# Kernel optimization log

Measured on AMD Instinct MI355X. Metric: run time of the kernel, lower is better.

Reference implementation:

```python
import jax, jax.numpy as jnp
import numpy as np

N = 8192   # nodes
D = 128    # uniform feature dim (arch = [128,128,128])
L = 2      # num_layers = len(arch)-1
EDGE_P = 0.01

def setup_inputs() -> dict:
    key = jax.random.key(0)
    ks = jax.random.split(key, 11)
    features = jax.random.normal(ks[0], (N, D), dtype=jnp.float32)
    # sparse symmetric adjacency with self-loops (diagonal forced True, as in forward)
    a = jax.random.uniform(ks[1], (N, N)) < EDGE_P
    mask = a | a.T | jnp.eye(N, dtype=bool)
    s = 1.0 / np.sqrt(D)
    def w(k):
        return (jax.random.normal(k, (L, D, D), dtype=jnp.float32) * s)
    def b(k):
        return jax.random.normal(k, (L, D), dtype=jnp.float32) * 0.01
    return {
        "features": features, "mask": mask,
        "Wq": w(ks[2]), "bq": b(ks[3]),
        "Wk": w(ks[4]), "bk": b(ks[5]),
        "Wv": w(ks[6]), "bv": b(ks[7]),
        "Wo": w(ks[8]), "bo": b(ks[9]),
    }

def reference(features, mask, Wq, bq, Wk, bk, Wv, bv, Wo, bo):
    h = features
    outputs = [h]
    for l in range(L):
        Q = h @ Wq[l] + bq[l]                      # [N, D]
        K = h @ Wk[l] + bk[l]
        V = h @ Wv[l] + bv[l]
        scores = (Q @ K.T) * (1.0 / jnp.sqrt(jnp.float32(K.shape[1])))  # [N, N]
        scores = jnp.where(mask, scores, -jnp.inf)
        attn = jax.nn.softmax(scores, axis=1)
        h = attn @ V                                # [N, D]
        h = h @ Wo[l] + bo[l]
        outputs.append(h)
    return tuple(outputs)
```

## Files before the change

kernel.cpp:

```cpp
#include <hip/hip_runtime.h>
#include <hip/hip_bf16.h>
#include <hip/hip_fp16.h>
#include <math.h>

#define N 8192
#define D 128
#define CAP 512

typedef _Float16 f16x2 __attribute__((ext_vector_type(2)));
typedef _Float16 f16x4 __attribute__((ext_vector_type(4)));
typedef _Float16 f16x8 __attribute__((ext_vector_type(8)));
typedef float    f32x4 __attribute__((ext_vector_type(4)));

__device__ __forceinline__ float dot2(f16x2 a, f16x2 b, float c) {
#if __has_builtin(__builtin_amdgcn_fdot2)
    return __builtin_amdgcn_fdot2(a, b, c, false);
#else
    return c + (float)a[0] * (float)b[0] + (float)a[1] * (float)b[1];
#endif
}

__device__ __forceinline__ float dot8(f16x8 a, f16x8 b) {
    float c0 = dot2(__builtin_shufflevector(a, a, 0, 1), __builtin_shufflevector(b, b, 0, 1), 0.f);
    float c1 = dot2(__builtin_shufflevector(a, a, 2, 3), __builtin_shufflevector(b, b, 2, 3), 0.f);
    c0 = dot2(__builtin_shufflevector(a, a, 4, 5), __builtin_shufflevector(b, b, 4, 5), c0);
    c1 = dot2(__builtin_shufflevector(a, a, 6, 7), __builtin_shufflevector(b, b, 6, 7), c1);
    return c0 + c1;
}

__global__ __launch_bounds__(256) void adj_qkv(const int* __restrict__ mask,
                                               unsigned short* __restrict__ nbr,
                                               int* __restrict__ deg,
                                               const float* __restrict__ A,
                                               const float* __restrict__ Wq, const float* __restrict__ bq,
                                               const float* __restrict__ Wk, const float* __restrict__ bk,
                                               const float* __restrict__ Wv, const float* __restrict__ bv,
                                               __half* __restrict__ Qo, __half* __restrict__ Ko,
                                               __half* __restrict__ Vo,
                                               float* __restrict__ copy_out) {
    __shared__ float As[8][D];
    const int tid = threadIdx.x;

    if (blockIdx.x < N) {
        const int i = blockIdx.x;
        __shared__ int cnt;
        if (tid == 0) cnt = 0;
        __syncthreads();
        const int4* row = (const int4*)(mask + (size_t)i * N);
        for (int c = tid; c < N / 4; c += 256) {
            int4 m4 = row[c];
            int base = 4 * c;
            if (m4.x) { int p = atomicAdd(&cnt, 1); if (p < CAP) nbr[(size_t)i * CAP + p] = (unsigned short)(base); }
            if (m4.y) { int p = atomicAdd(&cnt, 1); if (p < CAP) nbr[(size_t)i * CAP + p] = (unsigned short)(base + 1); }
            if (m4.z) { int p = atomicAdd(&cnt, 1); if (p < CAP) nbr[(size_t)i * CAP + p] = (unsigned short)(base + 2); }
            if (m4.w) { int p = atomicAdd(&cnt, 1); if (p < CAP) nbr[(size_t)i * CAP + p] = (unsigned short)(base + 3); }
        }
        __syncthreads();
        if (tid == 0) deg[i] = (cnt > CAP) ? CAP : cnt;
        return;
    }

    const int r   = tid >> 5;
    const int jg  = tid & 31;
    const int i0  = (blockIdx.x - N) * 8;

    const float4 av = ((const float4*)(A + (size_t)i0 * D))[tid];
    ((float4*)&As[0][0])[tid] = av;
    ((float4*)(copy_out + (size_t)i0 * D))[tid] = av;
    __syncthreads();

    const float* Ws[3] = {Wq, Wk, Wv};
    const float* bs[3] = {bq, bk, bv};
    __half* Os[3] = {Qo, Ko, Vo};
    const size_t st[3] = {D, 2 * D, 2 * D};

    #pragma unroll
    for (int m = 0; m < 3; ++m) {
        float4 acc = *(const float4*)(bs[m] + 4 * jg);
        const float* W = Ws[m];
        #pragma unroll 8
        for (int k4 = 0; k4 < 32; ++k4) {
            const float4 a4 = *(const float4*)&As[r][4 * k4];
            const float* wb = W + (size_t)(4 * k4) * D + 4 * jg;
            const float4 w0 = *(const float4*)(wb);
            const float4 w1 = *(const float4*)(wb + D);
            const float4 w2 = *(const float4*)(wb + 2 * D);
            const float4 w3 = *(const float4*)(wb + 3 * D);
            acc.x += a4.x * w0.x + a4.y * w1.x + a4.z * w2.x + a4.w * w3.x;
            acc.y += a4.x * w0.y + a4.y * w1.y + a4.z * w2.y + a4.w * w3.y;
            acc.z += a4.x * w0.z + a4.y * w1.z + a4.z * w2.z + a4.w * w3.z;
            acc.w += a4.x * w0.w + a4.y * w1.w + a4.z * w2.w + a4.w * w3.w;
        }
        f16x4 h;
        h[0] = (_Float16)acc.x; h[1] = (_Float16)acc.y;
        h[2] = (_Float16)acc.z; h[3] = (_Float16)acc.w;
        *(f16x4*)(Os[m] + (size_t)(i0 + r) * st[m] + 4 * jg) = h;
    }
}

__global__ __launch_bounds__(256) void gemmO_qkv(const float* __restrict__ Aattn,
                                                 const float* __restrict__ Wo, const float* __restrict__ bo,
                                                 float* __restrict__ Hout,
                                                 const float* __restrict__ Wq, const float* __restrict__ bq,
                                                 const float* __restrict__ Wk, const float* __restrict__ bk,
                                                 const float* __restrict__ Wv, const float* __restrict__ bv,
                                                 __half* __restrict__ Qo, __half* __restrict__ Ko,
                                                 __half* __restrict__ Vo) {
    __shared__ float As[8][D];
    __shared__ float Hs[8][D];
    const int tid = threadIdx.x;
    const int r   = tid >> 5;
    const int jg  = tid & 31;
    const int i0  = blockIdx.x * 8;

    ((float4*)&As[0][0])[tid] = ((const float4*)(Aattn + (size_t)i0 * D))[tid];
    __syncthreads();

    {
        float4 acc = *(const float4*)(bo + 4 * jg);
        #pragma unroll 8
        for (int k4 = 0; k4 < 32; ++k4) {
            const float4 a4 = *(const float4*)&As[r][4 * k4];
            const float* wb = Wo + (size_t)(4 * k4) * D + 4 * jg;
            const float4 w0 = *(const float4*)(wb);
            const float4 w1 = *(const float4*)(wb + D);
            const float4 w2 = *(const float4*)(wb + 2 * D);
            const float4 w3 = *(const float4*)(wb + 3 * D);
            acc.x += a4.x * w0.x + a4.y * w1.x + a4.z * w2.x + a4.w * w3.x;
            acc.y += a4.x * w0.y + a4.y * w1.y + a4.z * w2.y + a4.w * w3.y;
            acc.z += a4.x * w0.z + a4.y * w1.z + a4.z * w2.z + a4.w * w3.z;
            acc.w += a4.x * w0.w + a4.y * w1.w + a4.z * w2.w + a4.w * w3.w;
        }
        *(float4*)(Hout + (size_t)(i0 + r) * D + 4 * jg) = acc;
        *(float4*)&Hs[r][4 * jg] = acc;
    }
    __syncthreads();

    const float* Ws[3] = {Wq, Wk, Wv};
    const float* bs[3] = {bq, bk, bv};
    __half* Os[3] = {Qo, Ko, Vo};
    const size_t st[3] = {D, 2 * D, 2 * D};
    #pragma unroll
    for (int m = 0; m < 3; ++m) {
        float4 acc = *(const float4*)(bs[m] + 4 * jg);
        const float* W = Ws[m];
        #pragma unroll 8
        for (int k4 = 0; k4 < 32; ++k4) {
            const float4 a4 = *(const float4*)&Hs[r][4 * k4];
            const float* wb = W + (size_t)(4 * k4) * D + 4 * jg;
            const float4 w0 = *(const float4*)(wb);
            const float4 w1 = *(const float4*)(wb + D);
            const float4 w2 = *(const float4*)(wb + 2 * D);
            const float4 w3 = *(const float4*)(wb + 3 * D);
            acc.x += a4.x * w0.x + a4.y * w1.x + a4.z * w2.x + a4.w * w3.x;
            acc.y += a4.x * w0.y + a4.y * w1.y + a4.z * w2.y + a4.w * w3.y;
            acc.z += a4.x * w0.z + a4.y * w1.z + a4.z * w2.z + a4.w * w3.z;
            acc.w += a4.x * w0.w + a4.y * w1.w + a4.z * w2.w + a4.w * w3.w;
        }
        f16x4 h;
        h[0] = (_Float16)acc.x; h[1] = (_Float16)acc.y;
        h[2] = (_Float16)acc.z; h[3] = (_Float16)acc.w;
        *(f16x4*)(Os[m] + (size_t)(i0 + r) * st[m] + 4 * jg) = h;
    }
}

__global__ __launch_bounds__(256) void gemm_bias(const float* __restrict__ A,
                                                 const float* __restrict__ W,
                                                 const float* __restrict__ bias,
                                                 float* __restrict__ C) {
    __shared__ float As[8][D];
    const int tid = threadIdx.x;
    const int r   = tid >> 5;
    const int jg  = tid & 31;
    const int i0  = blockIdx.x * 8;

    ((float4*)&As[0][0])[tid] = ((const float4*)(A + (size_t)i0 * D))[tid];
    __syncthreads();

    float4 acc = *(const float4*)(bias + 4 * jg);
    #pragma unroll 8
    for (int k4 = 0; k4 < 32; ++k4) {
        const float4 a4 = *(const float4*)&As[r][4 * k4];
        const float* wb = W + (size_t)(4 * k4) * D + 4 * jg;
        const float4 w0 = *(const float4*)(wb);
        const float4 w1 = *(const float4*)(wb + D);
        const float4 w2 = *(const float4*)(wb + 2 * D);
        const float4 w3 = *(const float4*)(wb + 3 * D);
        acc.x += a4.x * w0.x + a4.y * w1.x + a4.z * w2.x + a4.w * w3.x;
        acc.y += a4.x * w0.y + a4.y * w1.y + a4.z * w2.y + a4.w * w3.y;
        acc.z += a4.x * w0.z + a4.y * w1.z + a4.z * w2.z + a4.w * w3.z;
        acc.w += a4.x * w0.w + a4.y * w1.w + a4.z * w2.w + a4.w * w3.w;
    }
    *(float4*)(C + (size_t)(i0 + r) * D + 4 * jg) = acc;
}

__global__ __launch_bounds__(256, 8) void attn_sparse(const __half* __restrict__ Q,
                                                      const __half* __restrict__ KV,
                                                      const unsigned short* __restrict__ nbr,
                                                      const int* __restrict__ deg,
                                                      float* __restrict__ Hout) {
    const int tid  = threadIdx.x;
    const int wave = tid >> 6;
    const int lane = tid & 63;
    const int g    = lane >> 4;
    const int gl   = lane & 15;
    const int i    = blockIdx.x * 4 + wave;

    __shared__ unsigned short jls[4][CAP];

    const int dg = min(deg[i], CAP);
    for (int e = lane; e < dg; e += 64)
        jls[wave][e] = __builtin_nontemporal_load(&nbr[(size_t)i * CAP + e]);
    const f16x8 qv = ((const f16x8*)(Q + (size_t)i * D))[gl];
    __syncthreads();

    const float scale = 0.088388347648318447f;

    float acc[8] = {0.f, 0.f, 0.f, 0.f, 0.f, 0.f, 0.f, 0.f};
    float denom  = 0.f;

    for (int e = g; e < dg; e += 4) {
        const int j = jls[wave][e];
        const f16x8* kvp = (const f16x8*)(KV + (size_t)j * (2 * D));
        const f16x8 kv = kvp[gl];
        const f16x8 v8 = kvp[16 + gl];
        float dot = dot8(kv, qv);
        dot += __shfl_xor(dot, 1);
        dot += __shfl_xor(dot, 2);
        dot += __shfl_xor(dot, 4);
        dot += __shfl_xor(dot, 8);
        const float p = __expf(dot * scale);
        #pragma unroll
        for (int k = 0; k < 8; ++k) acc[k] += p * (float)v8[k];
        denom += p;
    }

    #pragma unroll
    for (int k = 0; k < 8; ++k) {
        acc[k] += __shfl_xor(acc[k], 16);
        acc[k] += __shfl_xor(acc[k], 32);
    }
    denom += __shfl_xor(denom, 16);
    denom += __shfl_xor(denom, 32);

    if (g == 0) {
        const float inv = 1.0f / denom;
        f32x4 o0, o1;
        o0[0] = acc[0] * inv; o0[1] = acc[1] * inv; o0[2] = acc[2] * inv; o0[3] = acc[3] * inv;
        o1[0] = acc[4] * inv; o1[1] = acc[5] * inv; o1[2] = acc[6] * inv; o1[3] = acc[7] * inv;
        f32x4* dst = (f32x4*)(Hout + (size_t)i * D + 8 * gl);
        __builtin_nontemporal_store(o0, &dst[0]);
        __builtin_nontemporal_store(o1, &dst[1]);
    }
}

extern "C" void kernel_launch(void* const* d_in, const int* in_sizes, int n_in,
                              void* d_out, int out_size, void* d_ws, size_t ws_size,
                              hipStream_t stream) {
    const float* features = (const float*)d_in[0];
    const int*   mask     = (const int*)d_in[1];
    const float* Wq = (const float*)d_in[2];
    const float* bq = (const float*)d_in[3];
    const float* Wk = (const float*)d_in[4];
    const float* bk = (const float*)d_in[5];
    const float* Wv = (const float*)d_in[6];
    const float* bv = (const float*)d_in[7];
    const float* Wo = (const float*)d_in[8];
    const float* bo = (const float*)d_in[9];
    float* out = (float*)d_out;

    char* base = (char*)d_ws;
    unsigned short* nbr = (unsigned short*)base;
    int*    deg  = (int*)(base + (size_t)N * CAP * 2);
    __half* Qb16 = (__half*)(base + (size_t)N * CAP * 2 + N * 4);
    __half* KVb  = Qb16 + (size_t)N * D;
    float*  tmp  = (float*)(KVb + (size_t)N * 2 * D);

    adj_qkv<<<N + N / 8, 256, 0, stream>>>(mask, nbr, deg,
                                           features, Wq, bq, Wk, bk, Wv, bv,
                                           Qb16, KVb, KVb + D, out);
    attn_sparse<<<N / 4, 256, 0, stream>>>(Qb16, KVb, nbr, deg, tmp);
    gemmO_qkv<<<N / 8, 256, 0, stream>>>(tmp, Wo, bo, out + (size_t)N * D,
                                         Wq + D * D, bq + D, Wk + D * D, bk + D,
                                         Wv + D * D, bv + D, Qb16, KVb, KVb + D);
    attn_sparse<<<N / 4, 256, 0, stream>>>(Qb16, KVb, nbr, deg, tmp);
    gemm_bias<<<N / 8, 256, 0, stream>>>(tmp, Wo + D * D, bo + D,
                                         out + (size_t)2 * N * D);
}
```

Baseline: 569.3 us.

## Split sparse attention into two column-half passes for K/V cache locality

Neighbor lists are bucketed by whether the column lies in the first or second half of nodes, with per-half degrees. Attention runs as two passes, each gathering K/V only from one half so the working set per pass is halved and should hit cache more often. The first pass stores unnormalized partial sums and denominators, and the second combines and normalizes. This adds an extra kernel launch per layer and a global round trip for the partial accumulators, and caps each half at 256 neighbors.

```diff
diff --git a/kernel.cpp b/kernel.cpp
--- a/kernel.cpp
+++ b/kernel.cpp
@@ -6,6 +6,7 @@
 #define N 8192
 #define D 128
 #define CAP 512
+#define HCAP 256
 
 typedef _Float16 f16x2 __attribute__((ext_vector_type(2)));
 typedef _Float16 f16x4 __attribute__((ext_vector_type(4)));
@@ -30,7 +31,7 @@
 
 __global__ __launch_bounds__(256) void adj_qkv(const int* __restrict__ mask,
                                                unsigned short* __restrict__ nbr,
-                                               int* __restrict__ deg,
+                                               int* __restrict__ deg2,
                                                const float* __restrict__ A,
                                                const float* __restrict__ Wq, const float* __restrict__ bq,
                                                const float* __restrict__ Wk, const float* __restrict__ bk,
@@ -43,20 +44,22 @@
 
     if (blockIdx.x < N) {
         const int i = blockIdx.x;
-        __shared__ int cnt;
-        if (tid == 0) cnt = 0;
+        __shared__ int cnt2[2];
+        if (tid < 2) cnt2[tid] = 0;
         __syncthreads();
         const int4* row = (const int4*)(mask + (size_t)i * N);
         for (int c = tid; c < N / 4; c += 256) {
             int4 m4 = row[c];
             int base = 4 * c;
-            if (m4.x) { int p = atomicAdd(&cnt, 1); if (p < CAP) nbr[(size_t)i * CAP + p] = (unsigned short)(base); }
-            if (m4.y) { int p = atomicAdd(&cnt, 1); if (p < CAP) nbr[(size_t)i * CAP + p] = (unsigned short)(base + 1); }
-            if (m4.z) { int p = atomicAdd(&cnt, 1); if (p < CAP) nbr[(size_t)i * CAP + p] = (unsigned short)(base + 2); }
-            if (m4.w) { int p = atomicAdd(&cnt, 1); if (p < CAP) nbr[(size_t)i * CAP + p] = (unsigned short)(base + 3); }
+            int half = (base >= N / 2);
+            int boff = half * HCAP;
+            if (m4.x) { int p = atomicAdd(&cnt2[half], 1); if (p < HCAP) nbr[(size_t)i * CAP + boff + p] = (unsigned short)(base); }
+            if (m4.y) { int p = atomicAdd(&cnt2[half], 1); if (p < HCAP) nbr[(size_t)i * CAP + boff + p] = (unsigned short)(base + 1); }
+            if (m4.z) { int p = atomicAdd(&cnt2[half], 1); if (p < HCAP) nbr[(size_t)i * CAP + boff + p] = (unsigned short)(base + 2); }
+            if (m4.w) { int p = atomicAdd(&cnt2[half], 1); if (p < HCAP) nbr[(size_t)i * CAP + boff + p] = (unsigned short)(base + 3); }
         }
         __syncthreads();
-        if (tid == 0) deg[i] = (cnt > CAP) ? CAP : cnt;
+        if (tid < 2) deg2[2 * i + tid] = (cnt2[tid] > HCAP) ? HCAP : cnt2[tid];
         return;
     }
 
@@ -194,11 +197,14 @@
     *(float4*)(C + (size_t)(i0 + r) * D + 4 * jg) = acc;
 }
 
-__global__ __launch_bounds__(256, 8) void attn_sparse(const __half* __restrict__ Q,
-                                                      const __half* __restrict__ KV,
-                                                      const unsigned short* __restrict__ nbr,
-                                                      const int* __restrict__ deg,
-                                                      float* __restrict__ Hout) {
+template <int HALF>
+__global__ __launch_bounds__(256, 8) void attn_pass(const __half* __restrict__ Q,
+                                                    const __half* __restrict__ KV,
+                                                    const unsigned short* __restrict__ nbr,
+                                                    const int* __restrict__ deg2,
+                                                    float* __restrict__ Hacc,
+                                                    float* __restrict__ den,
+                                                    float* __restrict__ Hout) {
     const int tid  = threadIdx.x;
     const int wave = tid >> 6;
     const int lane = tid & 63;
@@ -206,12 +212,13 @@
     const int gl   = lane & 15;
     const int i    = blockIdx.x * 4 + wave;
 
-    __shared__ unsigned short jls[4][CAP];
-
-    const int dg = min(deg[i], CAP);
+    __shared__ unsigned short jls[4][HCAP];
+
+    const int dg = min(deg2[2 * i + HALF], HCAP);
+    const unsigned short* nb = nbr + (size_t)i * CAP + HALF * HCAP;
     for (int e = lane; e < dg; e += 64)
-        jls[wave][e] = __builtin_nontemporal_load(&nbr[(size_t)i * CAP + e]);
-    const f16x8 qv = ((const f16x8*)(Q + (size_t)i * D))[gl];
+        jls[wave][e] = __builtin_nontemporal_load(&nb[e]);
+    const f16x8 qv = __builtin_nontemporal_load(&((const f16x8*)(Q + (size_t)i * D))[gl]);
     __syncthreads();
 
     const float scale = 0.088388347648318447f;
@@ -243,14 +250,31 @@
     denom += __shfl_xor(denom, 16);
     denom += __shfl_xor(denom, 32);
 
-    if (g == 0) {
-        const float inv = 1.0f / denom;
-        f32x4 o0, o1;
-        o0[0] = acc[0] * inv; o0[1] = acc[1] * inv; o0[2] = acc[2] * inv; o0[3] = acc[3] * inv;
-        o1[0] = acc[4] * inv; o1[1] = acc[5] * inv; o1[2] = acc[6] * inv; o1[3] = acc[7] * inv;
-        f32x4* dst = (f32x4*)(Hout + (size_t)i * D + 8 * gl);
-        __builtin_nontemporal_store(o0, &dst[0]);
-        __builtin_nontemporal_store(o1, &dst[1]);
+    if constexpr (HALF == 0) {
+        if (g == 0) {
+            f32x4 o0, o1;
+            o0[0] = acc[0]; o0[1] = acc[1]; o0[2] = acc[2]; o0[3] = acc[3];
+            o1[0] = acc[4]; o1[1] = acc[5]; o1[2] = acc[6]; o1[3] = acc[7];
+            f32x4* dst = (f32x4*)(Hacc + (size_t)i * D + 8 * gl);
+            __builtin_nontemporal_store(o0, &dst[0]);
+            __builtin_nontemporal_store(o1, &dst[1]);
+        }
+        if (lane == 0) den[i] = denom;
+    } else {
+        if (g == 0) {
+            const f32x4* src = (const f32x4*)(Hacc + (size_t)i * D + 8 * gl);
+            const f32x4 a0 = __builtin_nontemporal_load(&src[0]);
+            const f32x4 a1 = __builtin_nontemporal_load(&src[1]);
+            const float inv = 1.0f / (denom + den[i]);
+            f32x4 o0, o1;
+            o0[0] = (acc[0] + a0[0]) * inv; o0[1] = (acc[1] + a0[1]) * inv;
+            o0[2] = (acc[2] + a0[2]) * inv; o0[3] = (acc[3] + a0[3]) * inv;
+            o1[0] = (acc[4] + a1[0]) * inv; o1[1] = (acc[5] + a1[1]) * inv;
+            o1[2] = (acc[6] + a1[2]) * inv; o1[3] = (acc[7] + a1[3]) * inv;
+            f32x4* dst = (f32x4*)(Hout + (size_t)i * D + 8 * gl);
+            __builtin_nontemporal_store(o0, &dst[0]);
+            __builtin_nontemporal_store(o1, &dst[1]);
+        }
     }
 }
 
@@ -271,19 +295,23 @@
 
     char* base = (char*)d_ws;
     unsigned short* nbr = (unsigned short*)base;
-    int*    deg  = (int*)(base + (size_t)N * CAP * 2);
-    __half* Qb16 = (__half*)(base + (size_t)N * CAP * 2 + N * 4);
+    int*    deg2 = (int*)(base + (size_t)N * CAP * 2);
+    float*  den  = (float*)(base + (size_t)N * CAP * 2 + 2 * N * 4);
+    __half* Qb16 = (__half*)(base + (size_t)N * CAP * 2 + 2 * N * 4 + N * 4);
     __half* KVb  = Qb16 + (size_t)N * D;
     float*  tmp  = (float*)(KVb + (size_t)N * 2 * D);
-
-    adj_qkv<<<N + N / 8, 256, 0, stream>>>(mask, nbr, deg,
+    float*  Hacc = out + (size_t)2 * N * D;
+
+    adj_qkv<<<N + N / 8, 256, 0, stream>>>(mask, nbr, deg2,
                                            features, Wq, bq, Wk, bk, Wv, bv,
                                            Qb16, KVb, KVb + D, out);
-    attn_sparse<<<N / 4, 256, 0, stream>>>(Qb16, KVb, nbr, deg, tmp);
+    attn_pass<0><<<N / 4, 256, 0, stream>>>(Qb16, KVb, nbr, deg2, Hacc, den, tmp);
+    attn_pass<1><<<N / 4, 256, 0, stream>>>(Qb16, KVb, nbr, deg2, Hacc, den, tmp);
     gemmO_qkv<<<N / 8, 256, 0, stream>>>(tmp, Wo, bo, out + (size_t)N * D,
                                          Wq + D * D, bq + D, Wk + D * D, bk + D,
                                          Wv + D * D, bv + D, Qb16, KVb, KVb + D);
-    attn_sparse<<<N / 4, 256, 0, stream>>>(Qb16, KVb, nbr, deg, tmp);
+    attn_pass<0><<<N / 4, 256, 0, stream>>>(Qb16, KVb, nbr, deg2, Hacc, den, tmp);
+    attn_pass<1><<<N / 4, 256, 0, stream>>>(Qb16, KVb, nbr, deg2, Hacc, den, tmp);
     gemm_bias<<<N / 8, 256, 0, stream>>>(tmp, Wo + D * D, bo + D,
                                          out + (size_t)2 * N * D);
 }
```

After: 584.2 us. 2.6% more time.

## Fuse output projection and next-layer QKV projection into sparse attention kernel

Applied to the files above, without the earlier changes.

The sparse attention kernel now also applies the Wo projection to each node's attention output. For the first layer it then computes the next layer's Q/K/V projections in the same kernel. This drops two separate GEMM launches and the fp32 intermediate round-trip through global memory. Each wave handles one row with a per-row matvec, so weight matrices are re-read once per 4-row block instead of once per 8-row block. Q/KV buffers are double-buffered to avoid overwriting inputs still being read by other blocks.

```diff
diff --git a/kernel.cpp b/kernel.cpp
--- a/kernel.cpp
+++ b/kernel.cpp
@@ -10,6 +10,7 @@
 typedef _Float16 f16x2 __attribute__((ext_vector_type(2)));
 typedef _Float16 f16x4 __attribute__((ext_vector_type(4)));
 typedef _Float16 f16x8 __attribute__((ext_vector_type(8)));
+typedef float    f32x2 __attribute__((ext_vector_type(2)));
 typedef float    f32x4 __attribute__((ext_vector_type(4)));
 
 __device__ __forceinline__ float dot2(f16x2 a, f16x2 b, float c) {
@@ -98,107 +99,18 @@
     }
 }
 
-__global__ __launch_bounds__(256) void gemmO_qkv(const float* __restrict__ Aattn,
-                                                 const float* __restrict__ Wo, const float* __restrict__ bo,
-                                                 float* __restrict__ Hout,
-                                                 const float* __restrict__ Wq, const float* __restrict__ bq,
-                                                 const float* __restrict__ Wk, const float* __restrict__ bk,
-                                                 const float* __restrict__ Wv, const float* __restrict__ bv,
-                                                 __half* __restrict__ Qo, __half* __restrict__ Ko,
-                                                 __half* __restrict__ Vo) {
-    __shared__ float As[8][D];
-    __shared__ float Hs[8][D];
-    const int tid = threadIdx.x;
-    const int r   = tid >> 5;
-    const int jg  = tid & 31;
-    const int i0  = blockIdx.x * 8;
-
-    ((float4*)&As[0][0])[tid] = ((const float4*)(Aattn + (size_t)i0 * D))[tid];
-    __syncthreads();
-
-    {
-        float4 acc = *(const float4*)(bo + 4 * jg);
-        #pragma unroll 8
-        for (int k4 = 0; k4 < 32; ++k4) {
-            const float4 a4 = *(const float4*)&As[r][4 * k4];
-            const float* wb = Wo + (size_t)(4 * k4) * D + 4 * jg;
-            const float4 w0 = *(const float4*)(wb);
-            const float4 w1 = *(const float4*)(wb + D);
-            const float4 w2 = *(const float4*)(wb + 2 * D);
-            const float4 w3 = *(const float4*)(wb + 3 * D);
-            acc.x += a4.x * w0.x + a4.y * w1.x + a4.z * w2.x + a4.w * w3.x;
-            acc.y += a4.x * w0.y + a4.y * w1.y + a4.z * w2.y + a4.w * w3.y;
-            acc.z += a4.x * w0.z + a4.y * w1.z + a4.z * w2.z + a4.w * w3.z;
-            acc.w += a4.x * w0.w + a4.y * w1.w + a4.z * w2.w + a4.w * w3.w;
-        }
-        *(float4*)(Hout + (size_t)(i0 + r) * D + 4 * jg) = acc;
-        *(float4*)&Hs[r][4 * jg] = acc;
-    }
-    __syncthreads();
-
-    const float* Ws[3] = {Wq, Wk, Wv};
-    const float* bs[3] = {bq, bk, bv};
-    __half* Os[3] = {Qo, Ko, Vo};
-    const size_t st[3] = {D, 2 * D, 2 * D};
-    #pragma unroll
-    for (int m = 0; m < 3; ++m) {
-        float4 acc = *(const float4*)(bs[m] + 4 * jg);
-        const float* W = Ws[m];
-        #pragma unroll 8
-        for (int k4 = 0; k4 < 32; ++k4) {
-            const float4 a4 = *(const float4*)&Hs[r][4 * k4];
-            const float* wb = W + (size_t)(4 * k4) * D + 4 * jg;
-            const float4 w0 = *(const float4*)(wb);
-            const float4 w1 = *(const float4*)(wb + D);
-            const float4 w2 = *(const float4*)(wb + 2 * D);
-            const float4 w3 = *(const float4*)(wb + 3 * D);
-            acc.x += a4.x * w0.x + a4.y * w1.x + a4.z * w2.x + a4.w * w3.x;
-            acc.y += a4.x * w0.y + a4.y * w1.y + a4.z * w2.y + a4.w * w3.y;
-            acc.z += a4.x * w0.z + a4.y * w1.z + a4.z * w2.z + a4.w * w3.z;
-            acc.w += a4.x * w0.w + a4.y * w1.w + a4.z * w2.w + a4.w * w3.w;
-        }
-        f16x4 h;
-        h[0] = (_Float16)acc.x; h[1] = (_Float16)acc.y;
-        h[2] = (_Float16)acc.z; h[3] = (_Float16)acc.w;
-        *(f16x4*)(Os[m] + (size_t)(i0 + r) * st[m] + 4 * jg) = h;
-    }
-}
-
-__global__ __launch_bounds__(256) void gemm_bias(const float* __restrict__ A,
-                                                 const float* __restrict__ W,
-                                                 const float* __restrict__ bias,
-                                                 float* __restrict__ C) {
-    __shared__ float As[8][D];
-    const int tid = threadIdx.x;
-    const int r   = tid >> 5;
-    const int jg  = tid & 31;
-    const int i0  = blockIdx.x * 8;
-
-    ((float4*)&As[0][0])[tid] = ((const float4*)(A + (size_t)i0 * D))[tid];
-    __syncthreads();
-
-    float4 acc = *(const float4*)(bias + 4 * jg);
-    #pragma unroll 8
-    for (int k4 = 0; k4 < 32; ++k4) {
-        const float4 a4 = *(const float4*)&As[r][4 * k4];
-        const float* wb = W + (size_t)(4 * k4) * D + 4 * jg;
-        const float4 w0 = *(const float4*)(wb);
-        const float4 w1 = *(const float4*)(wb + D);
-        const float4 w2 = *(const float4*)(wb + 2 * D);
-        const float4 w3 = *(const float4*)(wb + 3 * D);
-        acc.x += a4.x * w0.x + a4.y * w1.x + a4.z * w2.x + a4.w * w3.x;
-        acc.y += a4.x * w0.y + a4.y * w1.y + a4.z * w2.y + a4.w * w3.y;
-        acc.z += a4.x * w0.z + a4.y * w1.z + a4.z * w2.z + a4.w * w3.z;
-        acc.w += a4.x * w0.w + a4.y * w1.w + a4.z * w2.w + a4.w * w3.w;
-    }
-    *(float4*)(C + (size_t)(i0 + r) * D + 4 * jg) = acc;
-}
-
-__global__ __launch_bounds__(256, 8) void attn_sparse(const __half* __restrict__ Q,
+template <bool HAS_QKV>
+__global__ __launch_bounds__(256, 8) void fused_layer(const __half* __restrict__ Q,
                                                       const __half* __restrict__ KV,
                                                       const unsigned short* __restrict__ nbr,
                                                       const int* __restrict__ deg,
-                                                      float* __restrict__ Hout) {
+                                                      const float* __restrict__ Wo, const float* __restrict__ bo,
+                                                      float* __restrict__ Lout,
+                                                      const float* __restrict__ Wq, const float* __restrict__ bq,
+                                                      const float* __restrict__ Wk, const float* __restrict__ bk,
+                                                      const float* __restrict__ Wv, const float* __restrict__ bv,
+                                                      __half* __restrict__ Qout,
+                                                      __half* __restrict__ KVout) {
     const int tid  = threadIdx.x;
     const int wave = tid >> 6;
     const int lane = tid & 63;
@@ -207,6 +119,8 @@
     const int i    = blockIdx.x * 4 + wave;
 
     __shared__ unsigned short jls[4][CAP];
+    __shared__ float Hs[4][D];
+    __shared__ float Hs2[4][D];
 
     const int dg = min(deg[i], CAP);
     for (int e = lane; e < dg; e += 64)
@@ -243,14 +157,51 @@
     denom += __shfl_xor(denom, 16);
     denom += __shfl_xor(denom, 32);
 
+    const float inv = 1.0f / denom;
     if (g == 0) {
-        const float inv = 1.0f / denom;
-        f32x4 o0, o1;
-        o0[0] = acc[0] * inv; o0[1] = acc[1] * inv; o0[2] = acc[2] * inv; o0[3] = acc[3] * inv;
-        o1[0] = acc[4] * inv; o1[1] = acc[5] * inv; o1[2] = acc[6] * inv; o1[3] = acc[7] * inv;
-        f32x4* dst = (f32x4*)(Hout + (size_t)i * D + 8 * gl);
-        __builtin_nontemporal_store(o0, &dst[0]);
-        __builtin_nontemporal_store(o1, &dst[1]);
+        #pragma unroll
+        for (int k = 0; k < 8; ++k) Hs[wave][8 * gl + k] = acc[k] * inv;
+    }
+    __syncthreads();
+
+    const int c0 = 2 * lane;
+    float b0 = bo[c0], b1 = bo[c0 + 1];
+    #pragma unroll 4
+    for (int d = 0; d < D; ++d) {
+        const float hd = Hs[wave][d];
+        const f32x2 w = *(const f32x2*)(Wo + (size_t)d * D + c0);
+        b0 += hd * w[0];
+        b1 += hd * w[1];
+    }
+    {
+        f32x2 o; o[0] = b0; o[1] = b1;
+        *(f32x2*)(Lout + (size_t)i * D + c0) = o;
+    }
+
+    if constexpr (HAS_QKV) {
+        Hs2[wave][c0] = b0;
+        Hs2[wave][c0 + 1] = b1;
+        __syncthreads();
+
+        float aq0 = bq[c0], aq1 = bq[c0 + 1];
+        float ak0 = bk[c0], ak1 = bk[c0 + 1];
+        float av0 = bv[c0], av1 = bv[c0 + 1];
+        #pragma unroll 4
+        for (int d = 0; d < D; ++d) {
+            const float hd = Hs2[wave][d];
+            const f32x2 wq = *(const f32x2*)(Wq + (size_t)d * D + c0);
+            const f32x2 wk = *(const f32x2*)(Wk + (size_t)d * D + c0);
+            const f32x2 wv = *(const f32x2*)(Wv + (size_t)d * D + c0);
+            aq0 += hd * wq[0]; aq1 += hd * wq[1];
+            ak0 += hd * wk[0]; ak1 += hd * wk[1];
+            av0 += hd * wv[0]; av1 += hd * wv[1];
+        }
+        f16x2 hq; hq[0] = (_Float16)aq0; hq[1] = (_Float16)aq1;
+        f16x2 hk; hk[0] = (_Float16)ak0; hk[1] = (_Float16)ak1;
+        f16x2 hv; hv[0] = (_Float16)av0; hv[1] = (_Float16)av1;
+        *(f16x2*)(Qout + (size_t)i * D + c0) = hq;
+        *(f16x2*)(KVout + (size_t)i * (2 * D) + c0) = hk;
+        *(f16x2*)(KVout + (size_t)i * (2 * D) + D + c0) = hv;
     }
 }
 
@@ -272,18 +223,24 @@
     char* base = (char*)d_ws;
     unsigned short* nbr = (unsigned short*)base;
     int*    deg  = (int*)(base + (size_t)N * CAP * 2);
-    __half* Qb16 = (__half*)(base + (size_t)N * CAP * 2 + N * 4);
-    __half* KVb  = Qb16 + (size_t)N * D;
-    float*  tmp  = (float*)(KVb + (size_t)N * 2 * D);
+    __half* Q0   = (__half*)(base + (size_t)N * CAP * 2 + N * 4);
+    __half* KV0  = Q0 + (size_t)N * D;
+    __half* Q1   = KV0 + (size_t)N * 2 * D;
+    __half* KV1  = Q1 + (size_t)N * D;
 
     adj_qkv<<<N + N / 8, 256, 0, stream>>>(mask, nbr, deg,
                                            features, Wq, bq, Wk, bk, Wv, bv,
-                                           Qb16, KVb, KVb + D, out);
-    attn_sparse<<<N / 4, 256, 0, stream>>>(Qb16, KVb, nbr, deg, tmp);
-    gemmO_qkv<<<N / 8, 256, 0, stream>>>(tmp, Wo, bo, out + (size_t)N * D,
-                                         Wq + D * D, bq + D, Wk + D * D, bk + D,
-                                         Wv + D * D, bv + D, Qb16, KVb, KVb + D);
-    attn_sparse<<<N / 4, 256, 0, stream>>>(Qb16, KVb, nbr, deg, tmp);
-    gemm_bias<<<N / 8, 256, 0, stream>>>(tmp, Wo + D * D, bo + D,
-                                         out + (size_t)2 * N * D);
-}
+                                           Q0, KV0, KV0 + D, out);
+    fused_layer<true><<<N / 4, 256, 0, stream>>>(Q0, KV0, nbr, deg,
+                                                 Wo, bo, out + (size_t)N * D,
+                                                 Wq + D * D, bq + D,
+                                                 Wk + D * D, bk + D,
+                                                 Wv + D * D, bv + D,
+                                                 Q1, KV1);
+    fused_layer<false><<<N / 4, 256, 0, stream>>>(Q1, KV1, nbr, deg,
+                                                  Wo + D * D, bo + D,
+                                                  out + (size_t)2 * N * D,
+                                                  nullptr, nullptr, nullptr, nullptr,
+                                                  nullptr, nullptr,
+                                                  nullptr, nullptr);
+}
```

New measurement: 621.3 us. 1.09x slower.

## Replace sparse gather attention with dense bitmask MFMA flash attention

Applied to the files above, without the earlier changes.

Instead of building per-row neighbor lists and gathering K/V rows for each edge, the adjacency is packed into a bitmask via wave ballots, and attention is computed densely over all N keys with MFMA 16x16x32 f16 tiles, masking scores by bit lookup. The key range is split into two halves across blocks, with partial numerators and denominators combined and normalized in the following GEMM kernels. This trades about 50x more arithmetic (dense versus about 2% density) for regular tensor-core work and coalesced loads, and it launches only 256 blocks, which may underfill the GPU. Softmax skips max-subtraction, as before.

```diff
diff --git a/kernel.cpp b/kernel.cpp
--- a/kernel.cpp
+++ b/kernel.cpp
@@ -1,62 +1,39 @@
 #include <hip/hip_runtime.h>
-#include <hip/hip_bf16.h>
 #include <hip/hip_fp16.h>
 #include <math.h>
 
 #define N 8192
 #define D 128
-#define CAP 512
-
-typedef _Float16 f16x2 __attribute__((ext_vector_type(2)));
+
 typedef _Float16 f16x4 __attribute__((ext_vector_type(4)));
 typedef _Float16 f16x8 __attribute__((ext_vector_type(8)));
 typedef float    f32x4 __attribute__((ext_vector_type(4)));
 
-__device__ __forceinline__ float dot2(f16x2 a, f16x2 b, float c) {
-#if __has_builtin(__builtin_amdgcn_fdot2)
-    return __builtin_amdgcn_fdot2(a, b, c, false);
-#else
-    return c + (float)a[0] * (float)b[0] + (float)a[1] * (float)b[1];
-#endif
-}
-
-__device__ __forceinline__ float dot8(f16x8 a, f16x8 b) {
-    float c0 = dot2(__builtin_shufflevector(a, a, 0, 1), __builtin_shufflevector(b, b, 0, 1), 0.f);
-    float c1 = dot2(__builtin_shufflevector(a, a, 2, 3), __builtin_shufflevector(b, b, 2, 3), 0.f);
-    c0 = dot2(__builtin_shufflevector(a, a, 4, 5), __builtin_shufflevector(b, b, 4, 5), c0);
-    c1 = dot2(__builtin_shufflevector(a, a, 6, 7), __builtin_shufflevector(b, b, 6, 7), c1);
-    return c0 + c1;
-}
-
-__global__ __launch_bounds__(256) void adj_qkv(const int* __restrict__ mask,
-                                               unsigned short* __restrict__ nbr,
-                                               int* __restrict__ deg,
-                                               const float* __restrict__ A,
-                                               const float* __restrict__ Wq, const float* __restrict__ bq,
-                                               const float* __restrict__ Wk, const float* __restrict__ bk,
-                                               const float* __restrict__ Wv, const float* __restrict__ bv,
-                                               __half* __restrict__ Qo, __half* __restrict__ Ko,
-                                               __half* __restrict__ Vo,
-                                               float* __restrict__ copy_out) {
+__global__ __launch_bounds__(256) void bits_qkv(const int* __restrict__ mask,
+                                                unsigned* __restrict__ bits,
+                                                const float* __restrict__ A,
+                                                const float* __restrict__ Wq, const float* __restrict__ bq,
+                                                const float* __restrict__ Wk, const float* __restrict__ bk,
+                                                const float* __restrict__ Wv, const float* __restrict__ bv,
+                                                __half* __restrict__ Qo, __half* __restrict__ Ko,
+                                                __half* __restrict__ Vo,
+                                                float* __restrict__ copy_out) {
     __shared__ float As[8][D];
     const int tid = threadIdx.x;
 
     if (blockIdx.x < N) {
-        const int i = blockIdx.x;
-        __shared__ int cnt;
-        if (tid == 0) cnt = 0;
-        __syncthreads();
-        const int4* row = (const int4*)(mask + (size_t)i * N);
-        for (int c = tid; c < N / 4; c += 256) {
-            int4 m4 = row[c];
-            int base = 4 * c;
-            if (m4.x) { int p = atomicAdd(&cnt, 1); if (p < CAP) nbr[(size_t)i * CAP + p] = (unsigned short)(base); }
-            if (m4.y) { int p = atomicAdd(&cnt, 1); if (p < CAP) nbr[(size_t)i * CAP + p] = (unsigned short)(base + 1); }
-            if (m4.z) { int p = atomicAdd(&cnt, 1); if (p < CAP) nbr[(size_t)i * CAP + p] = (unsigned short)(base + 2); }
-            if (m4.w) { int p = atomicAdd(&cnt, 1); if (p < CAP) nbr[(size_t)i * CAP + p] = (unsigned short)(base + 3); }
-        }
-        __syncthreads();
-        if (tid == 0) deg[i] = (cnt > CAP) ? CAP : cnt;
+        const int i    = blockIdx.x;
+        const int wave = tid >> 6;
+        const int lane = tid & 63;
+        const unsigned* row = (const unsigned*)(mask + (size_t)i * N);
+        #pragma unroll 4
+        for (int c = 0; c < 32; ++c) {
+            const int base = c * 256 + wave * 64;
+            const unsigned w = row[base + lane];
+            const unsigned long long b = __ballot(w != 0);
+            if (lane == 0)
+                *(unsigned long long*)(bits + (size_t)i * 256 + (base >> 5)) = b;
+        }
         return;
     }
 
@@ -72,7 +49,6 @@
     const float* Ws[3] = {Wq, Wk, Wv};
     const float* bs[3] = {bq, bk, bv};
     __half* Os[3] = {Qo, Ko, Vo};
-    const size_t st[3] = {D, 2 * D, 2 * D};
 
     #pragma unroll
     for (int m = 0; m < 3; ++m) {
@@ -94,11 +70,121 @@
         f16x4 h;
         h[0] = (_Float16)acc.x; h[1] = (_Float16)acc.y;
         h[2] = (_Float16)acc.z; h[3] = (_Float16)acc.w;
-        *(f16x4*)(Os[m] + (size_t)(i0 + r) * st[m] + 4 * jg) = h;
-    }
-}
-
-__global__ __launch_bounds__(256) void gemmO_qkv(const float* __restrict__ Aattn,
+        *(f16x4*)(Os[m] + (size_t)(i0 + r) * D + 4 * jg) = h;
+    }
+}
+
+__global__ __launch_bounds__(256) void flash_attn(const __half* __restrict__ Q,
+                                                  const __half* __restrict__ K,
+                                                  const __half* __restrict__ V,
+                                                  const unsigned* __restrict__ bits,
+                                                  float* __restrict__ accP,
+                                                  float* __restrict__ denP) {
+    const int qt   = blockIdx.x >> 1;
+    const int h    = blockIdx.x & 1;
+    const int tid  = threadIdx.x;
+    const int wave = tid >> 6;
+    const int lane = tid & 63;
+    const int l15  = lane & 15;
+    const int lg   = lane >> 4;
+
+    __shared__ char lds[41472];
+    unsigned* mask_lds = (unsigned*)(lds + 40960);
+
+    const int qbase = qt * 64 + wave * 16;
+
+    f16x8 qf[4];
+    #pragma unroll
+    for (int c = 0; c < 4; ++c)
+        qf[c] = *(const f16x8*)(Q + (size_t)(qbase + l15) * D + c * 32 + lg * 8);
+
+    f32x4 Oacc[8];
+    #pragma unroll
+    for (int ds = 0; ds < 8; ++ds) Oacc[ds] = (f32x4){0.f, 0.f, 0.f, 0.f};
+    float den[4] = {0.f, 0.f, 0.f, 0.f};
+
+    const float scale = 0.088388347648318447f;
+
+    for (int t = 0; t < 64; ++t) {
+        const int kb = h * 4096 + t * 64;
+
+        #pragma unroll
+        for (int cc = 0; cc < 4; ++cc) {
+            const int idx  = tid + cc * 256;
+            const int krow = idx >> 4;
+            const int dp   = (idx & 15) * 8;
+            const f16x8 k8 = *(const f16x8*)(K + (size_t)(kb + krow) * D + dp);
+            *(f16x8*)(lds + ((krow * 256 + dp * 2) ^ ((krow & 7) << 4))) = k8;
+            const f16x8 v8 = *(const f16x8*)(V + (size_t)(kb + krow) * D + dp);
+            #pragma unroll
+            for (int e = 0; e < 8; ++e) {
+                const int d = dp + e;
+                *(_Float16*)(lds + 16384 + ((d * 128 + krow * 2) ^ ((d & 7) << 4))) = v8[e];
+            }
+        }
+        if (tid < 128)
+            mask_lds[tid] = bits[(size_t)(qt * 64 + (tid >> 1)) * 256 + (kb >> 5) + (tid & 1)];
+        __syncthreads();
+
+        #pragma unroll
+        for (int kt = 0; kt < 4; ++kt) {
+            f32x4 s = (f32x4){0.f, 0.f, 0.f, 0.f};
+            const int key = kt * 16 + l15;
+            #pragma unroll
+            for (int c = 0; c < 4; ++c) {
+                const f16x8 b = *(const f16x8*)(lds +
+                    ((key * 256 + (c * 32 + lg * 8) * 2) ^ ((key & 7) << 4)));
+                s = __builtin_amdgcn_mfma_f32_16x16x32_f16(qf[c], b, s, 0, 0, 0);
+            }
+            #pragma unroll
+            for (int r = 0; r < 4; ++r) {
+                const int q  = lg * 4 + r;
+                const unsigned mw = mask_lds[(wave * 16 + q) * 2 + (key >> 5)];
+                const float p = ((mw >> (key & 31)) & 1u) ? __expf(s[r] * scale) : 0.f;
+                den[r] += p;
+                *(_Float16*)(lds + 32768 + wave * 2048 +
+                             ((q * 128 + key * 2) ^ ((q & 7) << 4))) = (_Float16)p;
+            }
+        }
+
+        #pragma unroll
+        for (int kc = 0; kc < 2; ++kc) {
+            const f16x8 a = *(const f16x8*)(lds + 32768 + wave * 2048 +
+                ((l15 * 128 + (kc * 32 + lg * 8) * 2) ^ ((l15 & 7) << 4)));
+            #pragma unroll
+            for (int ds = 0; ds < 8; ++ds) {
+                const int d = ds * 16 + l15;
+                const f16x8 b = *(const f16x8*)(lds + 16384 +
+                    ((d * 128 + (kc * 32 + lg * 8) * 2) ^ ((d & 7) << 4)));
+                Oacc[ds] = __builtin_amdgcn_mfma_f32_16x16x32_f16(a, b, Oacc[ds], 0, 0, 0);
+            }
+        }
+        __syncthreads();
+    }
+
+    #pragma unroll
+    for (int r = 0; r < 4; ++r) {
+        den[r] += __shfl_xor(den[r], 1);
+        den[r] += __shfl_xor(den[r], 2);
+        den[r] += __shfl_xor(den[r], 4);
+        den[r] += __shfl_xor(den[r], 8);
+    }
+
+    float* ap = accP + (size_t)h * N * D;
+    #pragma unroll
+    for (int ds = 0; ds < 8; ++ds)
+        #pragma unroll
+        for (int r = 0; r < 4; ++r)
+            ap[(size_t)(qbase + lg * 4 + r) * D + ds * 16 + l15] = Oacc[ds][r];
+    if (l15 == 0) {
+        #pragma unroll
+        for (int r = 0; r < 4; ++r)
+            denP[h * N + qbase + lg * 4 + r] = den[r];
+    }
+}
+
+__global__ __launch_bounds__(256) void gemmO_qkv(const float* __restrict__ accP,
+                                                 const float* __restrict__ denP,
                                                  const float* __restrict__ Wo, const float* __restrict__ bo,
                                                  float* __restrict__ Hout,
                                                  const float* __restrict__ Wq, const float* __restrict__ bq,
@@ -113,7 +199,16 @@
     const int jg  = tid & 31;
     const int i0  = blockIdx.x * 8;
 
-    ((float4*)&As[0][0])[tid] = ((const float4*)(Aattn + (size_t)i0 * D))[tid];
+    {
+        const int i = i0 + (tid >> 5);
+        const float inv = 1.0f / (denP[i] + denP[N + i]);
+        const float4 a0 = ((const float4*)(accP + (size_t)i0 * D))[tid];
+        const float4 a1 = ((const float4*)(accP + (size_t)(N + i0) * D))[tid];
+        float4 v;
+        v.x = (a0.x + a1.x) * inv; v.y = (a0.y + a1.y) * inv;
+        v.z = (a0.z + a1.z) * inv; v.w = (a0.w + a1.w) * inv;
+        ((float4*)&As[0][0])[tid] = v;
+    }
     __syncthreads();
 
     {
@@ -139,7 +234,6 @@
     const float* Ws[3] = {Wq, Wk, Wv};
     const float* bs[3] = {bq, bk, bv};
     __half* Os[3] = {Qo, Ko, Vo};
-    const size_t st[3] = {D, 2 * D, 2 * D};
     #pragma unroll
     for (int m = 0; m < 3; ++m) {
         float4 acc = *(const float4*)(bs[m] + 4 * jg);
@@ -157,14 +251,15 @@
             acc.z += a4.x * w0.z + a4.y * w1.z + a4.z * w2.z + a4.w * w3.z;
             acc.w += a4.x * w0.w + a4.y * w1.w + a4.z * w2.w + a4.w * w3.w;
         }
-        f16x4 h;
-        h[0] = (_Float16)acc.x; h[1] = (_Float16)acc.y;
-        h[2] = (_Float16)acc.z; h[3] = (_Float16)acc.w;
-        *(f16x4*)(Os[m] + (size_t)(i0 + r) * st[m] + 4 * jg) = h;
-    }
-}
-
-__global__ __launch_bounds__(256) void gemm_bias(const float* __restrict__ A,
+        f16x4 hh;
+        hh[0] = (_Float16)acc.x; hh[1] = (_Float16)acc.y;
+        hh[2] = (_Float16)acc.z; hh[3] = (_Float16)acc.w;
+        *(f16x4*)(Os[m] + (size_t)(i0 + r) * D + 4 * jg) = hh;
+    }
+}
+
+__global__ __launch_bounds__(256) void gemm_bias(const float* __restrict__ accP,
+                                                 const float* __restrict__ denP,
                                                  const float* __restrict__ W,
                                                  const float* __restrict__ bias,
                                                  float* __restrict__ C) {
@@ -174,7 +269,16 @@
     const int jg  = tid & 31;
     const int i0  = blockIdx.x * 8;
 
-    ((float4*)&As[0][0])[tid] = ((const float4*)(A + (size_t)i0 * D))[tid];
+    {
+        const int i = i0 + (tid >> 5);
+        const float inv = 1.0f / (denP[i] + denP[N + i]);
+        const float4 a0 = ((const float4*)(accP + (size_t)i0 * D))[tid];
+        const float4 a1 = ((const float4*)(accP + (size_t)(N + i0) * D))[tid];
+        float4 v;
+        v.x = (a0.x + a1.x) * inv; v.y = (a0.y + a1.y) * inv;
+        v.z = (a0.z + a1.z) * inv; v.w = (a0.w + a1.w) * inv;
+        ((float4*)&As[0][0])[tid] = v;
+    }
     __syncthreads();
 
     float4 acc = *(const float4*)(bias + 4 * jg);
@@ -192,66 +296,6 @@
         acc.w += a4.x * w0.w + a4.y * w1.w + a4.z * w2.w + a4.w * w3.w;
     }
     *(float4*)(C + (size_t)(i0 + r) * D + 4 * jg) = acc;
-}
-
-__global__ __launch_bounds__(256, 8) void attn_sparse(const __half* __restrict__ Q,
-                                                      const __half* __restrict__ KV,
-                                                      const unsigned short* __restrict__ nbr,
-                                                      const int* __restrict__ deg,
-                                                      float* __restrict__ Hout) {
-    const int tid  = threadIdx.x;
-    const int wave = tid >> 6;
-    const int lane = tid & 63;
-    const int g    = lane >> 4;
-    const int gl   = lane & 15;
-    const int i    = blockIdx.x * 4 + wave;
-
-    __shared__ unsigned short jls[4][CAP];
-
-    const int dg = min(deg[i], CAP);
-    for (int e = lane; e < dg; e += 64)
-        jls[wave][e] = __builtin_nontemporal_load(&nbr[(size_t)i * CAP + e]);
-    const f16x8 qv = ((const f16x8*)(Q + (size_t)i * D))[gl];
-    __syncthreads();
-
-    const float scale = 0.088388347648318447f;
-
-    float acc[8] = {0.f, 0.f, 0.f, 0.f, 0.f, 0.f, 0.f, 0.f};
-    float denom  = 0.f;
-
-    for (int e = g; e < dg; e += 4) {
-        const int j = jls[wave][e];
-        const f16x8* kvp = (const f16x8*)(KV + (size_t)j * (2 * D));
-        const f16x8 kv = kvp[gl];
-        const f16x8 v8 = kvp[16 + gl];
-        float dot = dot8(kv, qv);
-        dot += __shfl_xor(dot, 1);
-        dot += __shfl_xor(dot, 2);
-        dot += __shfl_xor(dot, 4);
-        dot += __shfl_xor(dot, 8);
-        const float p = __expf(dot * scale);
-        #pragma unroll
-        for (int k = 0; k < 8; ++k) acc[k] += p * (float)v8[k];
-        denom += p;
-    }
-
-    #pragma unroll
-    for (int k = 0; k < 8; ++k) {
-        acc[k] += __shfl_xor(acc[k], 16);
-        acc[k] += __shfl_xor(acc[k], 32);
-    }
-    denom += __shfl_xor(denom, 16);
-    denom += __shfl_xor(denom, 32);
-
-    if (g == 0) {
-        const float inv = 1.0f / denom;
-        f32x4 o0, o1;
-        o0[0] = acc[0] * inv; o0[1] = acc[1] * inv; o0[2] = acc[2] * inv; o0[3] = acc[3] * inv;
-        o1[0] = acc[4] * inv; o1[1] = acc[5] * inv; o1[2] = acc[6] * inv; o1[3] = acc[7] * inv;
-        f32x4* dst = (f32x4*)(Hout + (size_t)i * D + 8 * gl);
-        __builtin_nontemporal_store(o0, &dst[0]);
-        __builtin_nontemporal_store(o1, &dst[1]);
-    }
 }
 
 extern "C" void kernel_launch(void* const* d_in, const int* in_sizes, int n_in,
@@ -270,20 +314,21 @@
     float* out = (float*)d_out;
 
     char* base = (char*)d_ws;
-    unsigned short* nbr = (unsigned short*)base;
-    int*    deg  = (int*)(base + (size_t)N * CAP * 2);
-    __half* Qb16 = (__half*)(base + (size_t)N * CAP * 2 + N * 4);
-    __half* KVb  = Qb16 + (size_t)N * D;
-    float*  tmp  = (float*)(KVb + (size_t)N * 2 * D);
-
-    adj_qkv<<<N + N / 8, 256, 0, stream>>>(mask, nbr, deg,
-                                           features, Wq, bq, Wk, bk, Wv, bv,
-                                           Qb16, KVb, KVb + D, out);
-    attn_sparse<<<N / 4, 256, 0, stream>>>(Qb16, KVb, nbr, deg, tmp);
-    gemmO_qkv<<<N / 8, 256, 0, stream>>>(tmp, Wo, bo, out + (size_t)N * D,
+    unsigned* bits = (unsigned*)base;
+    __half* Qf = (__half*)(base + (size_t)N * 256 * 4);
+    __half* Kf = Qf + (size_t)N * D;
+    __half* Vf = Kf + (size_t)N * D;
+    float* accP = (float*)(Vf + (size_t)N * D);
+    float* denP = accP + (size_t)2 * N * D;
+
+    bits_qkv<<<N + N / 8, 256, 0, stream>>>(mask, bits,
+                                            features, Wq, bq, Wk, bk, Wv, bv,
+                                            Qf, Kf, Vf, out);
+    flash_attn<<<256, 256, 0, stream>>>(Qf, Kf, Vf, bits, accP, denP);
+    gemmO_qkv<<<N / 8, 256, 0, stream>>>(accP, denP, Wo, bo, out + (size_t)N * D,
                                          Wq + D * D, bq + D, Wk + D * D, bk + D,
-                                         Wv + D * D, bv + D, Qb16, KVb, KVb + D);
-    attn_sparse<<<N / 4, 256, 0, stream>>>(Qb16, KVb, nbr, deg, tmp);
-    gemm_bias<<<N / 8, 256, 0, stream>>>(tmp, Wo + D * D, bo + D,
+                                         Wv + D * D, bv + D, Qf, Kf, Vf);
+    flash_attn<<<256, 256, 0, stream>>>(Qf, Kf, Vf, bits, accP, denP);
+    gemm_bias<<<N / 8, 256, 0, stream>>>(accP, denP, Wo + D * D, bo + D,
                                          out + (size_t)2 * N * D);
 }
```

Result: slower. 988.0 us (+73.5%).
